# Performance work log

Hardware: AMD Instinct MI355X
Metric: run time of the kernel (lower is better)

The kernel has to match this reference:

```python
import jax, jax.numpy as jnp
import numpy as np

E, B, T = 7, 50, 100               # ensemble (network_size), no_batches=50, time blocks
D, A, L, H, C = 128, 32, 256, 1024, 128  # data, action, latent, hidden, context sizes
H_STEP = 0.1                        # (t1 - t0) / T == dt -> one SDE step per block


def setup_inputs() -> dict:
    key = jax.random.key(0)
    ks = iter(jax.random.split(key, 64))
    def nrm(shape, scale=1.0):
        return jax.random.normal(next(ks), shape, jnp.float32) * scale
    def ens(i, o):
        s = 1.0 / np.sqrt(i)
        return nrm((E, i, o), s), nrm((E, o), s)
    def lin(i, o):
        s = 1.0 / np.sqrt(i)
        return nrm((i, o), s), nrm((o,), s)
    inp = {}
    inp["enc_w1"], inp["enc_b1"] = ens(D, H)
    inp["enc_w2"], inp["enc_b2"] = ens(H, H)
    inp["enc_w3"], inp["enc_b3"] = ens(H, C)
    inp["qz0_w"], inp["qz0_b"] = ens(C, 2 * L)
    inp["act_w"], inp["act_b"] = ens(L + A + D, L)
    inp["proj_w1"], inp["proj_b1"] = ens(L, H)
    inp["proj_w2"], inp["proj_b2"] = ens(H, H)
    inp["proj_w3"], inp["proj_b3"] = ens(H, D)
    inp["f_w1"], inp["f_b1"] = lin(L, H)
    inp["f_w2"], inp["f_b2"] = lin(H, H)
    inp["f_w3"], inp["f_b3"] = lin(H, L)
    inp["h_w1"], inp["h_b1"] = lin(L, H)
    inp["h_w2"], inp["h_b2"] = lin(H, H)
    inp["h_w3"], inp["h_b3"] = lin(H, L)
    # per-latent-dim g nets: Linear(1,H) -> ReLU -> Linear(H,1), stacked over L dims
    inp["g_w1"] = nrm((L, H), 0.2)
    inp["g_b1"] = nrm((L, H), 0.2)
    inp["g_w2"] = nrm((L, H), 0.2 / np.sqrt(H))
    inp["g_b2"] = 0.5 + nrm((L,), 0.01)   # keep diffusion bounded away from 0
    inp["pz0_mean"] = jnp.zeros((E, 1, L), jnp.float32)
    inp["pz0_logstd"] = jnp.zeros((E, 1, L), jnp.float32)
    inp["xs"] = nrm((E, T * B, D))
    inp["actions"] = nrm((E, T * B, A))
    inp["eps_z0"] = nrm((T, E, B, L))      # torch.randn_like noise for z0 reparam
    inp["dw_noise"] = nrm((T, E * B, L))   # Brownian increment noise (unit std)
    return inp


def reference(enc_w1, enc_b1, enc_w2, enc_b2, enc_w3, enc_b3,
              qz0_w, qz0_b, act_w, act_b,
              proj_w1, proj_b1, proj_w2, proj_b2, proj_w3, proj_b3,
              f_w1, f_b1, f_w2, f_b2, f_w3, f_b3,
              h_w1, h_b1, h_w2, h_b2, h_w3, h_b3,
              g_w1, g_b1, g_w2, g_b2,
              pz0_mean, pz0_logstd,
              xs, actions, eps_z0, dw_noise):
    def ens_lin(x, w, b):  # EnsembleFC: bmm + bias
        return jnp.einsum('ebi,eio->ebo', x, w) + b[:, None, :]

    def encoder(x):
        x = jax.nn.relu(ens_lin(x, enc_w1, enc_b1))
        x = jax.nn.relu(ens_lin(x, enc_w2, enc_b2))
        return ens_lin(x, enc_w3, enc_b3)

    def projector(z):
        z = jnp.tanh(ens_lin(z, proj_w1, proj_b1))
        z = jnp.tanh(ens_lin(z, proj_w2, proj_b2))
        return ens_lin(z, proj_w3, proj_b3)

    def mlp(y, w1, b1, w2, b2, w3, b3):  # Linear-ReLU-Linear-Tanh-Linear
        y = jax.nn.relu(y @ w1 + b1)
        y = jnp.tanh(y @ w2 + b2)
        return y @ w3 + b3

    def g_fn(y):  # vectorized per-dim tiny MLPs: y (N, L) -> (N, L)
        hh = jax.nn.relu(y[:, :, None] * g_w1[None] + g_b1[None])  # (N, L, H)
        return jnp.sum(hh * g_w2[None], axis=-1) + g_b2

    xs_t = jnp.moveaxis(xs.reshape(E, T, B, D), 1, 0)        # (T, E, B, D)
    act_t = jnp.moveaxis(actions.reshape(E, T, B, A), 1, 0)  # (T, E, B, A)
    sqrt_h = jnp.sqrt(jnp.float32(H_STEP))

    def step(carry, inps):
        zs_last, i = carry
        x_i, a_i, eps_i, dw_i = inps
        ctx = encoder(x_i)                                  # (E, B, C)
        q = ens_lin(ctx, qz0_w, qz0_b)                      # (E, B, 2L)
        qm, ql = q[..., :L], q[..., L:]
        z0 = qm + jnp.exp(ql) * eps_i
        z_in = jnp.where(i == 0, z0, zs_last)               # first step uses z0
        lad = jnp.concatenate([z_in, a_i, x_i], axis=2)
        z = ens_lin(lad, act_w, act_b).reshape(E * B, L)
        # one SDE step with logqp (f: posterior drift, h: prior drift, g: diffusion)
        fv = mlp(z, f_w1, f_b1, f_w2, f_b2, f_w3, f_b3)
        hv = mlp(z, h_w1, h_b1, h_w2, h_b2, h_w3, h_b3)
        gv = g_fn(z)
        u = (fv - hv) / gv
        lr = 0.5 * jnp.sum(u * u, axis=-1) * H_STEP         # (E*B,) log-ratio increment
        z_new = z + fv * H_STEP + gv * (sqrt_h * dw_i)
        zs_new = z_new.reshape(E, B, L)
        xm = projector(zs_new)                              # (E, B, D)
        # KL(q(z0) || p(z0)) for diagonal Gaussians
        kl = (pz0_logstd - ql) \
             + (jnp.exp(2.0 * ql) + (qm - pz0_mean) ** 2) / (2.0 * jnp.exp(2.0 * pz0_logstd)) \
             - 0.5
        logqp0 = kl.sum(axis=2).mean(axis=1)                # (E,)
        lr_mean = lr.reshape(E, B).mean(axis=1)             # (E,)
        return (zs_new, i + 1), (lr_mean, logqp0, xm)

    init = (jnp.zeros((E, B, L), xs.dtype), jnp.int32(0))
    (_, _), (lrm, lq0, xms) = jax.lax.scan(step, init, (xs_t, act_t, eps_z0, dw_noise))
    logqp_path = lrm.sum(axis=0) + lq0.sum(axis=0)          # (E,)
    predicted_xs = jnp.moveaxis(xms, 0, 1).reshape(E, T * B, D)
    return logqp_path, predicted_xs
```

## Files before the change

kernel.cpp:

```cpp
#include <hip/hip_runtime.h>
#include <hip/hip_bf16.h>
#include <math.h>

#define E_ 7
#define B_ 50
#define T_ 100
#define D_ 128
#define A_ 32
#define L_ 256
#define H_ 1024
#define C_ 128
#define EB_ 350
#define TB_ 5000
#define SQRTH 0.31622776601683794f

typedef __attribute__((ext_vector_type(8))) short s8v;
typedef __attribute__((ext_vector_type(4))) float f32x4;
typedef _Float16 f16x2 __attribute__((ext_vector_type(2)));
typedef __hip_bfloat16 bf16;

#define MFMA __builtin_amdgcn_mfma_f32_16x16x32_bf16

__device__ __forceinline__ int lswz(int row, int ck) {
  return ((ck & ~7) | ((ck ^ row) & 7)) << 3;
}

struct BG {
  const bf16* A[8];
  const bf16* W[8];
  const float* bias[8];
  float* Cf[8];
  bf16* Cb[8];
};

template<int BM, int ACT, int OUT>
__global__ __launch_bounds__(256)
void bgemm(BG g, int M, int K, int lda, int ldw, int ldc) {
  __shared__ short As[BM * 64];
  __shared__ short Ws[128 * 64];
  const short* Ap = (const short*)g.A[blockIdx.z];
  const short* Wp = (const short*)g.W[blockIdx.z];
  const int bm = blockIdx.x * BM, bn = blockIdx.y * 128;
  const int tid = threadIdx.x;
  const int wv = tid >> 6, lane = tid & 63;
  const int wm0 = (wv >> 1) * (BM / 2), wn0 = (wv & 1) * 64;
  const int l15 = lane & 15, l4 = lane >> 4;
  constexpr int FM = BM / 32;
  constexpr int AI = BM / 32;
  f32x4 acc[FM][4] = {};
  for (int k0 = 0; k0 < K; k0 += 64) {
    s8v av[AI], wvv[4];
#pragma unroll
    for (int i = 0; i < AI; ++i) {
      const int c = tid + i * 256, r = c >> 3, ck = c & 7;
      s8v v = {};
      if (bm + r < M) v = *(const s8v*)(Ap + (size_t)(bm + r) * lda + k0 + ck * 8);
      av[i] = v;
    }
#pragma unroll
    for (int i = 0; i < 4; ++i) {
      const int c = tid + i * 256, r = c >> 3, ck = c & 7;
      wvv[i] = *(const s8v*)(Wp + (size_t)(bn + r) * ldw + k0 + ck * 8);
    }
    __syncthreads();
#pragma unroll
    for (int i = 0; i < AI; ++i) {
      const int c = tid + i * 256, r = c >> 3, ck = c & 7;
      *(s8v*)(As + r * 64 + ((ck ^ (r & 7)) << 3)) = av[i];
    }
#pragma unroll
    for (int i = 0; i < 4; ++i) {
      const int c = tid + i * 256, r = c >> 3, ck = c & 7;
      *(s8v*)(Ws + r * 64 + ((ck ^ (r & 7)) << 3)) = wvv[i];
    }
    __syncthreads();
#pragma unroll
    for (int ks = 0; ks < 2; ++ks) {
// ... 68 lines not shown
    ((B4*)d)[i] = o;
  }
}

__global__ __launch_bounds__(256)
void packW(const float* __restrict__ src, bf16* __restrict__ dst, int K, int N) {
  const int idx = blockIdx.x * 256 + threadIdx.x;
  if (idx >= K * N) return;
  const int k = idx / N, n = idx - k * N;
  const size_t fo = ((size_t)(n >> 4) * (K >> 5) + (k >> 5)) * 512 +
                    (((k >> 3) & 3) << 7) + ((n & 15) << 3) + (k & 7);
  dst[fo] = __float2bfloat16(src[idx]);
}

__global__ __launch_bounds__(256)
void packWz(const float* __restrict__ act_w, bf16* __restrict__ hi, bf16* __restrict__ lo) {
  const int idx = blockIdx.x * 256 + threadIdx.x;
  if (idx >= E_ * 65536) return;
  const int e = idx >> 16, rem = idx & 65535, k = rem >> 8, n = rem & 255;
  const float w = act_w[(size_t)e * 416 * 256 + (size_t)k * 256 + n];
  const bf16 h = __float2bfloat16(w);
  const size_t fo = (size_t)e * 65536 + ((size_t)(n >> 4) * 8 + (k >> 5)) * 512 +
                    (((k >> 3) & 3) << 7) + ((n & 15) << 3) + (k & 7);
  hi[fo] = h;
  lo[fo] = __float2bfloat16(w - __bfloat162float(h));
}

__global__ __launch_bounds__(256)
void ax_build(const float* __restrict__ actions, const float* __restrict__ xs,
              bf16* __restrict__ dst) {
  const int idx = blockIdx.x * 256 + threadIdx.x;
  if (idx >= E_ * TB_ * 192) return;
  const int k = idx % 192;
  const int r = (idx / 192) % TB_;
  const int e = idx / (192 * TB_);
  float v = 0.f;
  if (k < 32) v = actions[((size_t)e * TB_ + r) * A_ + k];
  else if (k < 160) v = xs[((size_t)e * TB_ + r) * D_ + (k - 32)];
  dst[idx] = __float2bfloat16(v);
}

__global__ __launch_bounds__(256)
void waxT_build(const float* __restrict__ act_w, bf16* __restrict__ dst) {
  const int idx = blockIdx.x * 256 + threadIdx.x;
  if (idx >= E_ * 256 * 192) return;
  const int k = idx % 192;
  const int n = (idx / 192) % 256;
  const int e = idx / (192 * 256);
  float v = (k < 160) ? act_w[(size_t)e * 416 * 256 + (size_t)(256 + k) * 256 + n] : 0.f;
  dst[idx] = __float2bfloat16(v);
}

__global__ __launch_bounds__(256)
void gpack_build(const float* __restrict__ gw1, const float* __restrict__ gb1,
                 const float* __restrict__ gw2, _Float16* __restrict__ dst) {
  const int idx = blockIdx.x * 256 + threadIdx.x;
  if (idx >= 256 * 3 * 1024) return;
  const int l = idx / 3072, rem = idx - l * 3072, arr = rem >> 10, h = rem & 1023;
  const float* s = arr == 0 ? gw1 : (arr == 1 ? gb1 : gw2);
  dst[idx] = (_Float16)s[(size_t)l * 1024 + h];
}

__global__ __launch_bounds__(256)
void qkl_kernel(const float* __restrict__ ctx, int rows, int row_off, int ctx_estride,
                const float* __restrict__ qw, const float* __restrict__ qb,
                const float* __restrict__ pm, const float* __restrict__ pl,
                const float* __restrict__ eps0, bf16* __restrict__ z0hi,
                bf16* __restrict__ z0lo, float* __restrict__ logqp) {
  __shared__ float cx[16][128];
  __shared__ float red[16];
  const int e = blockIdx.y;
  const int r0 = blockIdx.x * 16;
  const int tid = threadIdx.x;
  {
    const int r = tid >> 4, c = (tid & 15) * 8;
    float4 v0 = make_float4(0.f, 0.f, 0.f, 0.f), v1 = v0;
    if (r0 + r < rows) {
      const float* src = ctx + (size_t)e * ctx_estride + (size_t)(r0 + r) * C_ + c;
      v0 = *(const float4*)src;
      v1 = *(const float4*)(src + 4);
    }
    *(float4*)&cx[r][c] = v0;
    *(float4*)&cx[r][c + 4] = v1;
  }
  if (tid < 16) red[tid] = 0.f;
  __syncthreads();
  const int j = tid;
  const float* w = qw + (size_t)e * C_ * 512;
  float am_[16] = {};
  float al_[16] = {};
  for (int k0 = 0; k0 < C_; k0 += 4) {
    float wm[4], wl[4];
#pragma unroll
    for (int q = 0; q < 4; ++q) {
      wm[q] = w[(size_t)(k0 + q) * 512 + j];
      wl[q] = w[(size_t)(k0 + q) * 512 + 256 + j];
    }
#pragma unroll
    for (int r = 0; r < 16; ++r) {
      const float4 cv = *(const float4*)&cx[r][k0];
      const float cc[4] = {cv.x, cv.y, cv.z, cv.w};
#pragma unroll
      for (int q = 0; q < 4; ++q) {
        am_[r] = fmaf(cc[q], wm[q], am_[r]);
        al_[r] = fmaf(cc[q], wl[q], al_[r]);
      }
    }
  }
  const float qbm = qb[(size_t)e * 512 + j];
  const float qbl = qb[(size_t)e * 512 + 256 + j];
  const float pmv = pm[(size_t)e * L_ + j];
  const float plv = pl[(size_t)e * L_ + j];
  const float inv2e = 0.5f * expf(-2.f * plv);
#pragma unroll
  for (int r = 0; r < 16; ++r) {
    float kl = 0.f;
    if (r0 + r < rows) {
      const float qm_ = am_[r] + qbm;
      const float ql_ = al_[r] + qbl;
      const float dm = qm_ - pmv;
      kl = plv - ql_ + (expf(2.f * ql_) + dm * dm) * inv2e - 0.5f;
      const int gi = row_off + r0 + r;
      if (gi < B_) {
        const size_t zi = ((size_t)e * B_ + gi) * L_ + j;
        const float z0 = qm_ + expf(ql_) * eps0[zi];
        const bf16 h = __float2bfloat16(z0);
        z0hi[zi] = h;
        z0lo[zi] = __float2bfloat16(z0 - __bfloat162float(h));
      }
    }
    for (int off = 32; off; off >>= 1) kl += __shfl_xor(kl, off, 64);
    if ((tid & 63) == 0) atomicAdd(&red[r], kl);
  }
  __syncthreads();
  if (tid < 16 && r0 + tid < rows) atomicAdd(&logqp[e], red[tid] * (1.0f / B_));
}

__global__ __launch_bounds__(256, 2)
void k1_act(const bf16* __restrict__ zhi, const bf16* __restrict__ zlo,
            const bf16* __restrict__ wzh, const bf16* __restrict__ wzl,
            const float* __restrict__ axw, float* __restrict__ zP,
            bf16* __restrict__ zPb, int t) {
  __shared__ short Ah[16 * 256];
  __shared__ short Al[16 * 256];
  const int e = blockIdx.z, rb = blockIdx.x, nb = blockIdx.y * 128;
  const int r0 = rb * 13;
  const int nrows = (50 - r0 < 13) ? (50 - r0) : 13;
  const int tid = threadIdx.x, lane = tid & 63, wv = tid >> 6;
  const int l15 = lane & 15, l4 = lane >> 4;
  const short* zh = (const short*)zhi + (size_t)(e * 50 + r0) * 256;
  const short* zl = (const short*)zlo + (size_t)(e * 50 + r0) * 256;
#pragma unroll
  for (int i = 0; i < 2; ++i) {
    const int lin = tid + i * 256, row = lin >> 5, ck = lin & 31;
    s8v vh = {}, vl = {};
    if (row < nrows) {
      vh = *(const s8v*)(zh + row * 256 + ck * 8);
      vl = *(const s8v*)(zl + row * 256 + ck * 8);
    }
    *(s8v*)(Ah + row * 256 + lswz(row, ck)) = vh;
    *(s8v*)(Al + row * 256 + lswz(row, ck)) = vl;
  }
  __syncthreads();
  const short* Bh = (const short*)wzh + (size_t)e * 65536;
  const short* Bl = (const short*)wzl + (size_t)e * 65536;
  f32x4 acc[2] = {};
#pragma unroll
  for (int kt = 0; kt < 8; ++kt) {
    const int ck = kt * 4 + l4;
    const s8v ah = *(const s8v*)(Ah + l15 * 256 + lswz(l15, ck));
    const s8v al = *(const s8v*)(Al + l15 * 256 + lswz(l15, ck));
#pragma unroll
    for (int nt = 0; nt < 2; ++nt) {
      const int ng = nb + wv * 32 + nt * 16;
      const size_t bo = ((size_t)(ng >> 4) * 8 + kt) * 512 + lane * 8;
      const s8v bh = *(const s8v*)(Bh + bo);
      const s8v bl = *(const s8v*)(Bl + bo);
      acc[nt] = MFMA(ah, bh, acc[nt], 0, 0, 0);
      acc[nt] = MFMA(al, bh, acc[nt], 0, 0, 0);
      acc[nt] = MFMA(ah, bl, acc[nt], 0, 0, 0);
    }
  }
#pragma unroll
  for (int nt = 0; nt < 2; ++nt) {
    const int col = nb + wv * 32 + nt * 16 + l15;
#pragma unroll
    for (int j = 0; j < 4; ++j) {
      const int row = l4 * 4 + j;
      if (row < nrows) {
        const int gr = e * 50 + r0 + row;
        const float v = acc[nt][j] + axw[((size_t)e * TB_ + t * 50 + r0 + row) * 256 + col];
        zP[(size_t)gr * 256 + col] = v;
        zPb[(size_t)gr * 256 + col] = __float2bfloat16(v);
      }
    }
  }
}

__global__ __launch_bounds__(256, 2)
void k2_l1(const bf16* __restrict__ zPb, const bf16* __restrict__ w1f,
           const float* __restrict__ fb1, const float* __restrict__ hb1,
           bf16* __restrict__ fh1) {
  __shared__ short As[16 * 256];
  const int rb = blockIdx.x, nb = blockIdx.y * 128;
  const int r0 = rb * 16;
  const int tid = threadIdx.x, lane = tid & 63, wv = tid >> 6;
  const int l15 = lane & 15, l4 = lane >> 4;
#pragma unroll
  for (int i = 0; i < 2; ++i) {
    const int lin = tid + i * 256, row = lin >> 5, ck = lin & 31;
    s8v v = {};
    if (r0 + row < EB_)
      v = *(const s8v*)((const short*)zPb + (size_t)(r0 + row) * 256 + ck * 8);
    *(s8v*)(As + row * 256 + lswz(row, ck)) = v;
  }
  __syncthreads();
  f32x4 acc[2] = {};
#pragma unroll
  for (int kt = 0; kt < 8; ++kt) {
    const int ck = kt * 4 + l4;
    const s8v a = *(const s8v*)(As + l15 * 256 + lswz(l15, ck));
#pragma unroll
    for (int nt = 0; nt < 2; ++nt) {
      const int ng = nb + wv * 32 + nt * 16;
      const s8v b = *(const s8v*)((const short*)w1f + ((size_t)(ng >> 4) * 8 + kt) * 512 + lane * 8);
      acc[nt] = MFMA(a, b, acc[nt], 0, 0, 0);
    }
  }
#pragma unroll
  for (int nt = 0; nt < 2; ++nt) {
    const int col = nb + wv * 32 + nt * 16 + l15;
    const float bv = (col < 1024) ? fb1[col] : hb1[col - 1024];
#pragma unroll
    for (int j = 0; j < 4; ++j) {
      const int row = r0 + l4 * 4 + j;
      if (row < EB_)
        fh1[(size_t)row * 2048 + col] = __float2bfloat16(fmaxf(acc[nt][j] + bv, 0.f));
    }
  }
}

__global__ __launch_bounds__(256, 2)
void k3_l2(const bf16* __restrict__ fh1, const bf16* __restrict__ w2f,
           const float* __restrict__ fb2, const float* __restrict__ hb2,
           bf16* __restrict__ fh2) {
  __shared__ short As[16 * 1024];
  const int rb = blockIdx.x, nbl = blockIdx.y;
  const int nb = nbl * 128, r0 = rb * 16;
  const int half = (nbl >= 8) ? 1024 : 0;
  const int tid = threadIdx.x, lane = tid & 63, wv = tid >> 6;
  const int l15 = lane & 15, l4 = lane >> 4;
#pragma unroll
  for (int i = 0; i < 8; ++i) {
    const int lin = tid + i * 256, row = lin >> 7, ck = lin & 127;
    s8v v = {};
    if (r0 + row < EB_)
      v = *(const s8v*)((const short*)fh1 + (size_t)(r0 + row) * 2048 + half + ck * 8);
    *(s8v*)(As + row * 1024 + lswz(row, ck)) = v;
  }
  __syncthreads();
  f32x4 acc[2] = {};
#pragma unroll 4
  for (int kt = 0; kt < 32; ++kt) {
    const int ck = kt * 4 + l4;
    const s8v a = *(const s8v*)(As + l15 * 1024 + lswz(l15, ck));
#pragma unroll
    for (int nt = 0; nt < 2; ++nt) {
      const int ng = nb + wv * 32 + nt * 16;
      const s8v b = *(const s8v*)((const short*)w2f + ((size_t)(ng >> 4) * 32 + kt) * 512 + lane * 8);
      acc[nt] = MFMA(a, b, acc[nt], 0, 0, 0);
    }
  }
#pragma unroll
  for (int nt = 0; nt < 2; ++nt) {
    const int col = nb + wv * 32 + nt * 16 + l15;
    const float bv = half ? hb2[col - 1024] : fb2[col];
#pragma unroll
    for (int j = 0; j < 4; ++j) {
      const int row = r0 + l4 * 4 + j;
      if (row < EB_)
        fh2[(size_t)row * 2048 + col] = __float2bfloat16(tanhf(acc[nt][j] + bv));
    }
  }
}

__global__ __launch_bounds__(256, 1)
void k4_fin(const bf16* __restrict__ fh2, const bf16* __restrict__ w3f,
            const float* __restrict__ fb3, const float* __restrict__ hb3,
            const _Float16* __restrict__ gpk, const float* __restrict__ gb2,
            const float* __restrict__ zP, const float* __restrict__ dw,
            bf16* __restrict__ zhi, bf16* __restrict__ zlo,
            bf16* __restrict__ zs_bf, float* __restrict__ logqp, int t) {
  __shared__ short As[16 * 1024];
  __shared__ float ztile[16][64];
  __shared__ float gvt[16][64];
  __shared__ float ebuck[8];
  const int rb = blockIdx.x, cb = blockIdx.y;
  const int r0 = rb * 16, c0 = cb * 64;
  const int tid = threadIdx.x, lane = tid & 63, wv = tid >> 6;
  const int l15 = lane & 15, l4 = lane >> 4;
  if (tid < 8) ebuck[tid] = 0.f;
#pragma unroll
  for (int i = 0; i < 4; ++i) {
    const int lin = tid + i * 256, row = lin >> 6, col = lin & 63;
    ztile[row][col] = (r0 + row < EB_) ? zP[(size_t)(r0 + row) * 256 + c0 + col] : 1.0f;
  }
  f32x4 accF = {}, accH = {};
#pragma unroll
  for (int fb = 0; fb < 2; ++fb) {
    __syncthreads();
#pragma unroll
    for (int i = 0; i < 8; ++i) {
      const int lin = tid + i * 256, row = lin >> 7, ck = lin & 127;
      s8v v = {};
      if (r0 + row < EB_)
        v = *(const s8v*)((const short*)fh2 + (size_t)(r0 + row) * 2048 + fb * 1024 + ck * 8);
      *(s8v*)(As + row * 1024 + lswz(row, ck)) = v;
    }
    __syncthreads();
    const int ng = fb * 256 + c0 + wv * 16;
    f32x4 acc = {};
#pragma unroll 4
    for (int kt = 0; kt < 32; ++kt) {
      const int ck = kt * 4 + l4;
      const s8v a = *(const s8v*)(As + l15 * 1024 + lswz(l15, ck));
      const s8v b = *(const s8v*)((const short*)w3f + ((size_t)(ng >> 4) * 32 + kt) * 512 + lane * 8);
      acc = MFMA(a, b, acc, 0, 0, 0);
    }
    if (fb) accH = acc; else accF = acc;
  }
  __syncthreads();
  {
    const int lloc = tid >> 2, hq = tid & 3;
    const _Float16* gl = gpk + (size_t)(c0 + lloc) * 3072 + hq * 256;
    f16x2 z2[16];
#pragma unroll
    for (int r = 0; r < 16; ++r) {
      const _Float16 zh_ = (_Float16)ztile[r][lloc];
      z2[r] = f16x2{zh_, zh_};
    }
    float ga[16] = {};
    for (int hp = 0; hp < 128; ++hp) {
      const f16x2 w1v = *(const f16x2*)(gl + 2 * hp);
      const f16x2 b1v = *(const f16x2*)(gl + 1024 + 2 * hp);
      const f16x2 w2v = *(const f16x2*)(gl + 2048 + 2 * hp);
#pragma unroll
      for (int r = 0; r < 16; ++r) {
        f16x2 tt = z2[r] * w1v + b1v;
#if __has_builtin(__builtin_elementwise_max)
        const f16x2 zz = {};
        tt = __builtin_elementwise_max(tt, zz);
#else
        tt[0] = tt[0] > (_Float16)0 ? tt[0] : (_Float16)0;
        tt[1] = tt[1] > (_Float16)0 ? tt[1] : (_Float16)0;
#endif
#if __has_builtin(__builtin_amdgcn_fdot2)
        ga[r] = __builtin_amdgcn_fdot2(tt, w2v, ga[r], false);
#else
        ga[r] += (float)tt[0] * (float)w2v[0] + (float)tt[1] * (float)w2v[1];
#endif
      }
    }
#pragma unroll
    for (int r = 0; r < 16; ++r) {
      float v = ga[r];
      v += __shfl_xor(v, 1, 64);
      v += __shfl_xor(v, 2, 64);
      if (hq == 0) gvt[r][lloc] = v + gb2[c0 + lloc];
    }
  }
  __syncthreads();
  const int col_loc = wv * 16 + l15, col = c0 + col_loc;
  const float fb3v = fb3[col], hb3v = hb3[col];
#pragma unroll
  for (int j = 0; j < 4; ++j) {
    const int rl = l4 * 4 + j, row = r0 + rl;
    if (row < EB_) {
      const float fv = accF[j] + fb3v;
      const float hv = accH[j] + hb3v;
      const float gv = gvt[rl][col_loc];
      const float u = (fv - hv) / gv;
      atomicAdd(&ebuck[row / 50], 0.001f * u * u);
      const float znew = ztile[rl][col_loc] + 0.1f * fv +
                         gv * (SQRTH * dw[(size_t)t * (EB_ * 256) + (size_t)row * 256 + col]);
      const bf16 h = __float2bfloat16(znew);
      const size_t zi = (size_t)row * 256 + col;
      zhi[zi] = h;
      zlo[zi] = __float2bfloat16(znew - __bfloat162float(h));
      const int e = row / 50, b = row - e * 50;
      zs_bf[((size_t)e * TB_ + t * 50 + b) * 256 + col] = h;
    }
  }
  __syncthreads();
  if (tid < 7) {
    const float v = ebuck[tid];
    if (v != 0.f) atomicAdd(&logqp[tid], v);
  }
}

__global__ void init_kernel(float* logqp) {
  if (threadIdx.x < E_) logqp[threadIdx.x] = 0.f;
}

extern "C" void kernel_launch(void* const* d_in, const int* in_sizes, int n_in,
                              void* d_out, int out_size, void* d_ws, size_t ws_size,
                              hipStream_t stream) {
  (void)in_sizes; (void)n_in; (void)out_size;
  const float* enc_w1 = (const float*)d_in[0];
  const float* enc_b1 = (const float*)d_in[1];
  const float* enc_w2 = (const float*)d_in[2];
  const float* enc_b2 = (const float*)d_in[3];
  const float* enc_w3 = (const float*)d_in[4];
  const float* enc_b3 = (const float*)d_in[5];
  const float* qz0_w  = (const float*)d_in[6];
  const float* qz0_b  = (const float*)d_in[7];
  const float* act_w  = (const float*)d_in[8];
  const float* act_b  = (const float*)d_in[9];
  const float* proj_w1 = (const float*)d_in[10];
  const float* proj_b1 = (const float*)d_in[11];
  const float* proj_w2 = (const float*)d_in[12];
  const float* proj_b2 = (const float*)d_in[13];
  const float* proj_w3 = (const float*)d_in[14];
  const float* proj_b3 = (const float*)d_in[15];
  const float* f_w1 = (const float*)d_in[16];
  const float* f_b1 = (const float*)d_in[17];
  const float* f_w2 = (const float*)d_in[18];
  const float* f_b2 = (const float*)d_in[19];
  const float* f_w3 = (const float*)d_in[20];
  const float* f_b3 = (const float*)d_in[21];
  const float* h_w1 = (const float*)d_in[22];
  const float* h_b1 = (const float*)d_in[23];
  const float* h_w2 = (const float*)d_in[24];
  const float* h_b2 = (const float*)d_in[25];
  const float* h_w3 = (const float*)d_in[26];
  const float* h_b3 = (const float*)d_in[27];
  const float* g_w1 = (const float*)d_in[28];
  const float* g_b1 = (const float*)d_in[29];
  const float* g_w2 = (const float*)d_in[30];
  const float* g_b2 = (const float*)d_in[31];
  const float* pz0_mean   = (const float*)d_in[32];
  const float* pz0_logstd = (const float*)d_in[33];
  const float* xs      = (const float*)d_in[34];
  const float* actions = (const float*)d_in[35];
  const float* eps_z0  = (const float*)d_in[36];
  const float* dw      = (const float*)d_in[37];

  float* out = (float*)d_out;
  float* logqp = out;
  float* pred = out + E_;

  char* base = (char*)d_ws;
  size_t off = 0;
  auto alloc = [&](size_t bytes) {
    void* p = base + off;
    off = (off + bytes + 255) & ~(size_t)255;
    return p;
  };
  bf16* zhi    = (bf16*)alloc((size_t)EB_ * 256 * 2);
  bf16* zlo    = (bf16*)alloc((size_t)EB_ * 256 * 2);
  float* zP    = (float*)alloc((size_t)EB_ * 256 * 4);
  bf16* zPb    = (bf16*)alloc((size_t)EB_ * 256 * 2);
  bf16* fh1    = (bf16*)alloc((size_t)EB_ * 2048 * 2);
  bf16* fh2    = (bf16*)alloc((size_t)EB_ * 2048 * 2);
  bf16* zs_bf  = (bf16*)alloc((size_t)E_ * T_ * B_ * 256 * 2);
  float* axw   = (float*)alloc((size_t)E_ * TB_ * 256 * 4);
  bf16* ax_bf  = (bf16*)alloc((size_t)E_ * TB_ * 192 * 2);
  bf16* waxT   = (bf16*)alloc((size_t)E_ * 256 * 192 * 2);
  bf16* wzh    = (bf16*)alloc((size_t)E_ * 65536 * 2);
  bf16* wzl    = (bf16*)alloc((size_t)E_ * 65536 * 2);
  bf16* w1f    = (bf16*)alloc((size_t)2048 * 256 * 2);
  bf16* w2f    = (bf16*)alloc((size_t)2048 * 1024 * 2);
  bf16* w3f    = (bf16*)alloc((size_t)512 * 1024 * 2);
  _Float16* gpk = (_Float16*)alloc((size_t)256 * 3 * 1024 * 2);
  bf16* xs_bf  = (bf16*)alloc((size_t)E_ * TB_ * D_ * 2);
  bf16* ew1T = (bf16*)alloc((size_t)E_ * D_ * H_ * 2);
  bf16* ew2T = (bf16*)alloc((size_t)E_ * H_ * H_ * 2);
  bf16* ew3T = (bf16*)alloc((size_t)E_ * H_ * C_ * 2);
  bf16* pw1T = (bf16*)alloc((size_t)E_ * L_ * H_ * 2);
  bf16* pw2T = (bf16*)alloc((size_t)E_ * H_ * H_ * 2);
  bf16* pw3T = (bf16*)alloc((size_t)E_ * H_ * D_ * 2);
  const size_t per_row = (size_t)E_ * (H_ * 2 * 2 + C_ * 4);
  size_t remain = (ws_size > off + 4096) ? (ws_size - off - 4096) : 0;
  int CH = (int)(remain / per_row);
  if (CH > 2500) CH = 2500;
  if (CH < 64) CH = 64;
  bf16* bufA = (bf16*)alloc((size_t)E_ * CH * H_ * 2);
  bf16* bufB = (bf16*)alloc((size_t)E_ * CH * H_ * 2);
  float* bufC = (float*)alloc((size_t)E_ * CH * C_ * 4);

  init_kernel<<<dim3(1), dim3(64), 0, stream>>>(logqp);

  const dim3 cb256(256);
  cvt_kernel<<<dim3((E_ * TB_ * D_ / 4 + 255) / 256), cb256, 0, stream>>>(xs, xs_bf, E_ * TB_ * D_ / 4);
  cvtT_kernel<<<dim3(H_ / 32, D_ / 32, E_), cb256, 0, stream>>>(enc_w1, ew1T, D_, H_, (long)D_ * H_, (long)D_ * H_);
  cvtT_kernel<<<dim3(H_ / 32, H_ / 32, E_), cb256, 0, stream>>>(enc_w2, ew2T, H_, H_, (long)H_ * H_, (long)H_ * H_);
  cvtT_kernel<<<dim3(C_ / 32, H_ / 32, E_), cb256, 0, stream>>>(enc_w3, ew3T, H_, C_, (long)H_ * C_, (long)H_ * C_);
  cvtT_kernel<<<dim3(H_ / 32, L_ / 32, E_), cb256, 0, stream>>>(proj_w1, pw1T, L_, H_, (long)L_ * H_, (long)L_ * H_);
  cvtT_kernel<<<dim3(H_ / 32, H_ / 32, E_), cb256, 0, stream>>>(proj_w2, pw2T, H_, H_, (long)H_ * H_, (long)H_ * H_);
  cvtT_kernel<<<dim3(D_ / 32, H_ / 32, E_), cb256, 0, stream>>>(proj_w3, pw3T, H_, D_, (long)H_ * D_, (long)H_ * D_);
  ax_build<<<dim3((E_ * TB_ * 192 + 255) / 256), cb256, 0, stream>>>(actions, xs, ax_bf);
  waxT_build<<<dim3((E_ * 256 * 192 + 255) / 256), cb256, 0, stream>>>(act_w, waxT);
  packWz<<<dim3((E_ * 65536 + 255) / 256), cb256, 0, stream>>>(act_w, wzh, wzl);
  packW<<<dim3((256 * 1024 + 255) / 256), cb256, 0, stream>>>(f_w1, w1f, 256, 1024);
  packW<<<dim3((256 * 1024 + 255) / 256), cb256, 0, stream>>>(h_w1, w1f + (size_t)1024 * 256, 256, 1024);
  packW<<<dim3((1024 * 1024 + 255) / 256), cb256, 0, stream>>>(f_w2, w2f, 1024, 1024);
  packW<<<dim3((1024 * 1024 + 255) / 256), cb256, 0, stream>>>(h_w2, w2f + (size_t)1024 * 1024, 1024, 1024);
  packW<<<dim3((1024 * 256 + 255) / 256), cb256, 0, stream>>>(f_w3, w3f, 1024, 256);
  packW<<<dim3((1024 * 256 + 255) / 256), cb256, 0, stream>>>(h_w3, w3f + (size_t)256 * 1024, 1024, 256);
  gpack_build<<<dim3((256 * 3 * 1024 + 255) / 256), cb256, 0, stream>>>(g_w1, g_b1, g_w2, gpk);

  BG g;
  for (int e = 0; e < E_; ++e) {
    g.A[e] = ax_bf + (size_t)e * TB_ * 192;
    g.W[e] = waxT + (size_t)e * 256 * 192;
    g.bias[e] = act_b + (size_t)e * 256;
    g.Cf[e] = axw + (size_t)e * TB_ * 256;
  }
  bgemm<128, 0, 0><<<dim3((TB_ + 127) / 128, 2, E_), 256, 0, stream>>>(g, TB_, 192, 192, 192, 256);

  for (int c = 0; c < TB_; c += CH) {
    const int rows = (TB_ - c < CH) ? (TB_ - c) : CH;
    const int mt = (rows + 127) / 128;
    for (int e = 0; e < E_; ++e) {
      g.A[e] = xs_bf + ((size_t)e * TB_ + c) * D_;
      g.W[e] = ew1T + (size_t)e * D_ * H_;
      g.bias[e] = enc_b1 + (size_t)e * H_;
      g.Cb[e] = bufA + (size_t)e * CH * H_;
    }
    bgemm<128, 1, 1><<<dim3(mt, H_ / 128, E_), 256, 0, stream>>>(g, rows, D_, D_, D_, H_);
    for (int e = 0; e < E_; ++e) {
      g.A[e] = bufA + (size_t)e * CH * H_;
      g.W[e] = ew2T + (size_t)e * H_ * H_;
      g.bias[e] = enc_b2 + (size_t)e * H_;
      g.Cb[e] = bufB + (size_t)e * CH * H_;
    }
    bgemm<128, 1, 1><<<dim3(mt, H_ / 128, E_), 256, 0, stream>>>(g, rows, H_, H_, H_, H_);
    for (int e = 0; e < E_; ++e) {
      g.A[e] = bufB + (size_t)e * CH * H_;
      g.W[e] = ew3T + (size_t)e * H_ * C_;
      g.bias[e] = enc_b3 + (size_t)e * C_;
      g.Cf[e] = bufC + (size_t)e * CH * C_;
    }
    bgemm<128, 0, 0><<<dim3(mt, C_ / 128, E_), 256, 0, stream>>>(g, rows, H_, H_, H_, C_);
    qkl_kernel<<<dim3((rows + 15) / 16, E_), 256, 0, stream>>>(
        bufC, rows, c, CH * C_, qz0_w, qz0_b, pz0_mean, pz0_logstd, eps_z0,
        zhi, zlo, logqp);
  }

  for (int t = 0; t < T_; ++t) {
    k1_act<<<dim3(4, 2, E_), 256, 0, stream>>>(zhi, zlo, wzh, wzl, axw, zP, zPb, t);
    k2_l1<<<dim3(22, 16), 256, 0, stream>>>(zPb, w1f, f_b1, h_b1, fh1);
    k3_l2<<<dim3(22, 16), 256, 0, stream>>>(fh1, w2f, f_b2, h_b2, fh2);
    k4_fin<<<dim3(22, 4), 256, 0, stream>>>(fh2, w3f, f_b3, h_b3, gpk, g_b2,
                                            zP, dw, zhi, zlo, zs_bf, logqp, t);
  }

  for (int c = 0; c < TB_; c += CH) {
    const int rows = (TB_ - c < CH) ? (TB_ - c) : CH;
    const int mt = (rows + 127) / 128;
    for (int e = 0; e < E_; ++e) {
      g.A[e] = zs_bf + ((size_t)e * T_ * B_ + c) * L_;
      g.W[e] = pw1T + (size_t)e * L_ * H_;
      g.bias[e] = proj_b1 + (size_t)e * H_;
      g.Cb[e] = bufA + (size_t)e * CH * H_;
    }
    bgemm<128, 2, 1><<<dim3(mt, H_ / 128, E_), 256, 0, stream>>>(g, rows, L_, L_, L_, H_);
    for (int e = 0; e < E_; ++e) {
      g.A[e] = bufA + (size_t)e * CH * H_;
      g.W[e] = pw2T + (size_t)e * H_ * H_;
      g.bias[e] = proj_b2 + (size_t)e * H_;
      g.Cb[e] = bufB + (size_t)e * CH * H_;
    }
    bgemm<128, 2, 1><<<dim3(mt, H_ / 128, E_), 256, 0, stream>>>(g, rows, H_, H_, H_, H_);
    for (int e = 0; e < E_; ++e) {
      g.A[e] = bufB + (size_t)e * CH * H_;
      g.W[e] = pw3T + (size_t)e * H_ * D_;
      g.bias[e] = proj_b3 + (size_t)e * D_;
      g.Cf[e] = pred + ((size_t)e * TB_ + c) * D_;
    }
    bgemm<128, 0, 0><<<dim3(mt, D_ / 128, E_), 256, 0, stream>>>(g, rows, H_, H_, H_, D_);
  }
}
```

Baseline: 10.30 ms.

## Fuse SDE time loop into single persistent kernel with warp-specialized g-net

The 400 per-step launches (act, layer1, layer2, final) are replaced by one persistent kernel of 28 workgroups, one per ensemble member and batch quarter, which keeps the latent state in LDS across all 100 steps. Eight waves run the f and h MLPs on MFMA while the other eight compute the per-dimension g-net in fp16 concurrently. The g weights are repacked for coalesced access, and the z state is held in fp32 in LDS instead of being written back to global as hi/lo bf16 each step. This removes launch overhead and global round-trips, at the cost of using only 28 CUs and each workgroup re-streaming the full f/h weights from cache every step.

```diff
diff --git a/kernel.cpp b/kernel.cpp
--- a/kernel.cpp
+++ b/kernel.cpp
@@ -22,7 +22,28 @@
 #define MFMA __builtin_amdgcn_mfma_f32_16x16x32_bf16
 
 __device__ __forceinline__ int lswz(int row, int ck) {
-  return ((ck & ~7) | ((ck ^ row) & 7)) << 3;
+  return (((ck & ~7) | ((ck ^ row) & 7)) << 3);
+}
+__device__ __forceinline__ int swzE(int r, int col) {
+  const int ck = col >> 3;
+  return (((ck & ~7) | ((ck ^ r) & 7)) << 3) + (col & 7);
+}
+__device__ __forceinline__ f16x2 relu2(f16x2 t) {
+#if __has_builtin(__builtin_elementwise_max)
+  const f16x2 zz = {};
+  return __builtin_elementwise_max(t, zz);
+#else
+  t[0] = t[0] > (_Float16)0 ? t[0] : (_Float16)0;
+  t[1] = t[1] > (_Float16)0 ? t[1] : (_Float16)0;
+  return t;
+#endif
+}
+__device__ __forceinline__ float fdot2a(f16x2 a, f16x2 b, float c) {
+#if __has_builtin(__builtin_amdgcn_fdot2)
+  return __builtin_amdgcn_fdot2(a, b, c, false);
+#else
+  return c + (float)a[0] * (float)b[0] + (float)a[1] * (float)b[1];
+#endif
 }
 
 struct BG {
@@ -197,21 +218,24 @@
 }
 
 __global__ __launch_bounds__(256)
-void gpack_build(const float* __restrict__ gw1, const float* __restrict__ gb1,
-                 const float* __restrict__ gw2, _Float16* __restrict__ dst) {
+void gpack2(const float* __restrict__ gw1, const float* __restrict__ gb1,
+            const float* __restrict__ gw2, _Float16* __restrict__ dst) {
   const int idx = blockIdx.x * 256 + threadIdx.x;
-  if (idx >= 256 * 3 * 1024) return;
-  const int l = idx / 3072, rem = idx - l * 3072, arr = rem >> 10, h = rem & 1023;
+  if (idx >= 3 * 512 * 256 * 2) return;
+  const int i = idx & 1;
+  const int l = (idx >> 1) & 255;
+  const int hpg = (idx >> 9) & 511;
+  const int arr = idx >> 18;
   const float* s = arr == 0 ? gw1 : (arr == 1 ? gb1 : gw2);
-  dst[idx] = (_Float16)s[(size_t)l * 1024 + h];
+  dst[idx] = (_Float16)s[(size_t)l * 1024 + hpg * 2 + i];
 }
 
 __global__ __launch_bounds__(256)
 void qkl_kernel(const float* __restrict__ ctx, int rows, int row_off, int ctx_estride,
                 const float* __restrict__ qw, const float* __restrict__ qb,
                 const float* __restrict__ pm, const float* __restrict__ pl,
-                const float* __restrict__ eps0, bf16* __restrict__ z0hi,
-                bf16* __restrict__ z0lo, float* __restrict__ logqp) {
+                const float* __restrict__ eps0, float* __restrict__ z0f,
+                float* __restrict__ logqp) {
   __shared__ float cx[16][128];
   __shared__ float red[16];
   const int e = blockIdx.y;
@@ -268,10 +292,7 @@
       const int gi = row_off + r0 + r;
       if (gi < B_) {
         const size_t zi = ((size_t)e * B_ + gi) * L_ + j;
-        const float z0 = qm_ + expf(ql_) * eps0[zi];
-        const bf16 h = __float2bfloat16(z0);
-        z0hi[zi] = h;
-        z0lo[zi] = __float2bfloat16(z0 - __bfloat162float(h));
+        z0f[zi] = qm_ + expf(ql_) * eps0[zi];
       }
     }
     for (int off = 32; off; off >>= 1) kl += __shfl_xor(kl, off, 64);
@@ -281,265 +302,258 @@
   if (tid < 16 && r0 + tid < rows) atomicAdd(&logqp[e], red[tid] * (1.0f / B_));
 }
 
-__global__ __launch_bounds__(256, 2)
-void k1_act(const bf16* __restrict__ zhi, const bf16* __restrict__ zlo,
-            const bf16* __restrict__ wzh, const bf16* __restrict__ wzl,
-            const float* __restrict__ axw, float* __restrict__ zP,
-            bf16* __restrict__ zPb, int t) {
-  __shared__ short Ah[16 * 256];
-  __shared__ short Al[16 * 256];
-  const int e = blockIdx.z, rb = blockIdx.x, nb = blockIdx.y * 128;
-  const int r0 = rb * 13;
-  const int nrows = (50 - r0 < 13) ? (50 - r0) : 13;
-  const int tid = threadIdx.x, lane = tid & 63, wv = tid >> 6;
+struct SC {
+  const bf16 *wzh, *wzl, *w1f, *w2f, *w3f;
+  const _Float16* gpk;
+  const float *fb1, *hb1, *fb2, *hb2, *fb3, *hb3, *gb2;
+  const float *axw, *dw, *z0f;
+  bf16* zs_bf;
+  float* logqp;
+};
+
+template<int KT, int NT>
+__device__ __forceinline__ void mm(const short* As_, int astride, const short* Bf,
+                                   int ngBase, int lane, f32x4* acc) {
   const int l15 = lane & 15, l4 = lane >> 4;
-  const short* zh = (const short*)zhi + (size_t)(e * 50 + r0) * 256;
-  const short* zl = (const short*)zlo + (size_t)(e * 50 + r0) * 256;
-#pragma unroll
-  for (int i = 0; i < 2; ++i) {
-    const int lin = tid + i * 256, row = lin >> 5, ck = lin & 31;
-    s8v vh = {}, vl = {};
-    if (row < nrows) {
-      vh = *(const s8v*)(zh + row * 256 + ck * 8);
-      vl = *(const s8v*)(zl + row * 256 + ck * 8);
-    }
-    *(s8v*)(Ah + row * 256 + lswz(row, ck)) = vh;
-    *(s8v*)(Al + row * 256 + lswz(row, ck)) = vl;
+#pragma unroll 4
+  for (int kt = 0; kt < KT; ++kt) {
+    const s8v av = *(const s8v*)(As_ + l15 * astride + lswz(l15, kt * 4 + l4));
+#pragma unroll
+    for (int nt = 0; nt < NT; ++nt) {
+      const s8v bv = *(const s8v*)(Bf + ((size_t)((ngBase + nt) * KT + kt)) * 512 + lane * 8);
+      acc[nt] = MFMA(av, bv, acc[nt], 0, 0, 0);
+    }
+  }
+}
+
+__global__ __launch_bounds__(1024, 4) void scan28(SC a) {
+  __shared__ float zst[16 * 256];
+  __shared__ float zP[16 * 256];
+  __shared__ float fvb[16 * 256];
+  __shared__ float gvt[16 * 256];
+  __shared__ short zPb[16 * 256];
+  __shared__ short zh_[16 * 256];
+  __shared__ short zl_[16 * 256];
+  __shared__ short S[16 * 1024];
+  __shared__ short S2[16 * 1024];
+  const int wg = blockIdx.x;
+  const int e = wg >> 2, q = wg & 3;
+  const int nr = (q < 2) ? 13 : 12;
+  const int b0 = (q < 2) ? q * 13 : 26 + (q - 2) * 12;
+  const int tid = threadIdx.x;
+  const int wave = tid >> 6, lane = tid & 63, l15 = lane & 15, l4 = lane >> 4;
+  const int mw = wave & 7;
+  const bool isM = wave < 8;
+  const int gt = (wave - 8) * 64 + lane;
+  const int gl = gt >> 1, ghh = gt & 1;
+
+  for (int i = tid; i < 4096; i += 1024) {
+    const int r = i >> 8, c = i & 255;
+    zst[i] = (r < nr) ? a.z0f[(size_t)((e * 50 + b0 + r) * 256 + c)] : 0.f;
+  }
+  float lrA = 0.f;
+  const short* wzhE = (const short*)a.wzh + (size_t)e * 65536;
+  const short* wzlE = (const short*)a.wzl + (size_t)e * 65536;
+  const short* w1p = (const short*)a.w1f;
+  const short* w2p = (const short*)a.w2f;
+  const short* w3p = (const short*)a.w3f;
+
+  for (int t = 0; t < T_; ++t) {
+    __syncthreads();
+    for (int i = tid; i < 4096; i += 1024) {
+      const int r = i >> 8, c = i & 255;
+      const float f = zst[i];
+      const bf16 h = __float2bfloat16(f);
+      const bf16 lo = __float2bfloat16(f - __bfloat162float(h));
+      const int eo = r * 256 + swzE(r, c);
+      *(bf16*)&zh_[eo] = h;
+      *(bf16*)&zl_[eo] = lo;
+    }
+    __syncthreads();
+    {
+      f32x4 acc = {};
+#pragma unroll
+      for (int kt = 0; kt < 8; ++kt) {
+        const s8v ah = *(const s8v*)(zh_ + l15 * 256 + lswz(l15, kt * 4 + l4));
+        const s8v al = *(const s8v*)(zl_ + l15 * 256 + lswz(l15, kt * 4 + l4));
+        const size_t bo = ((size_t)(wave * 8 + kt)) * 512 + lane * 8;
+        const s8v bh = *(const s8v*)(wzhE + bo);
+        const s8v bl = *(const s8v*)(wzlE + bo);
+        acc = MFMA(ah, bh, acc, 0, 0, 0);
+        acc = MFMA(al, bh, acc, 0, 0, 0);
+        acc = MFMA(ah, bl, acc, 0, 0, 0);
+      }
+      const int col = wave * 16 + l15;
+#pragma unroll
+      for (int j = 0; j < 4; ++j) {
+        const int r = l4 * 4 + j;
+        float v = 0.f;
+        if (r < nr)
+          v = acc[j] + a.axw[((size_t)(e * TB_) + t * 50 + b0 + r) * 256 + col];
+        zP[r * 256 + col] = v;
+        *(bf16*)&zPb[r * 256 + swzE(r, col)] = __float2bfloat16(v);
+      }
+    }
+    __syncthreads();
+
+    f16x2 z2g[13];
+    float ga[13];
+    if (!isM) {
+#pragma unroll
+      for (int r = 0; r < 13; ++r) {
+        const _Float16 zh2 = (_Float16)zP[r * 256 + gl];
+        z2g[r] = f16x2{zh2, zh2};
+        ga[r] = 0.f;
+      }
+    }
+    auto gchunk = [&](int h0, int h1) {
+      for (int hp = h0; hp < h1; ++hp) {
+        const size_t o = ((size_t)(ghh * 256 + hp)) * 512 + gl * 2;
+        const f16x2 w1 = *(const f16x2*)(a.gpk + o);
+        const f16x2 b1 = *(const f16x2*)(a.gpk + 262144 + o);
+        const f16x2 w2 = *(const f16x2*)(a.gpk + 524288 + o);
+#pragma unroll
+        for (int r = 0; r < 13; ++r)
+          ga[r] = fdot2a(relu2(z2g[r] * w1 + b1), w2, ga[r]);
+      }
+    };
+
+    if (isM) {
+#pragma unroll
+      for (int ph = 0; ph < 2; ++ph) {
+        f32x4 acc[4] = {};
+        mm<8, 4>(zPb, 256, w1p, mw * 8 + ph * 4, lane, acc);
+#pragma unroll
+        for (int nt = 0; nt < 4; ++nt) {
+          const int col = (mw * 8 + ph * 4 + nt) * 16 + l15;
+          const float bv = a.fb1[col];
+#pragma unroll
+          for (int j = 0; j < 4; ++j) {
+            const int r = l4 * 4 + j;
+            *(bf16*)&S[r * 1024 + swzE(r, col)] =
+                __float2bfloat16(fmaxf(acc[nt][j] + bv, 0.f));
+          }
+        }
+      }
+    } else gchunk(0, 24);
+    __syncthreads();
+    if (isM) {
+#pragma unroll
+      for (int ph = 0; ph < 2; ++ph) {
+        f32x4 acc[4] = {};
+        mm<32, 4>(S, 1024, w2p, mw * 8 + ph * 4, lane, acc);
+#pragma unroll
+        for (int nt = 0; nt < 4; ++nt) {
+          const int col = (mw * 8 + ph * 4 + nt) * 16 + l15;
+          const float bv = a.fb2[col];
+#pragma unroll
+          for (int j = 0; j < 4; ++j) {
+            const int r = l4 * 4 + j;
+            *(bf16*)&S2[r * 1024 + swzE(r, col)] =
+                __float2bfloat16(tanhf(acc[nt][j] + bv));
+          }
+        }
+      }
+    } else gchunk(24, 104);
+    __syncthreads();
+    if (isM) {
+      f32x4 acc[2] = {};
+      mm<32, 2>(S2, 1024, w3p, mw * 2, lane, acc);
+#pragma unroll
+      for (int nt = 0; nt < 2; ++nt) {
+        const int col = (mw * 2 + nt) * 16 + l15;
+        const float bv = a.fb3[col];
+#pragma unroll
+        for (int j = 0; j < 4; ++j)
+          fvb[(l4 * 4 + j) * 256 + col] = acc[nt][j] + bv;
+      }
+    } else gchunk(104, 128);
+    __syncthreads();
+    if (isM) {
+#pragma unroll
+      for (int ph = 0; ph < 2; ++ph) {
+        f32x4 acc[4] = {};
+        mm<8, 4>(zPb, 256, w1p, 64 + mw * 8 + ph * 4, lane, acc);
+#pragma unroll
+        for (int nt = 0; nt < 4; ++nt) {
+          const int col = (mw * 8 + ph * 4 + nt) * 16 + l15;
+          const float bv = a.hb1[col];
+#pragma unroll
+          for (int j = 0; j < 4; ++j) {
+            const int r = l4 * 4 + j;
+            *(bf16*)&S[r * 1024 + swzE(r, col)] =
+                __float2bfloat16(fmaxf(acc[nt][j] + bv, 0.f));
+          }
+        }
+      }
+    } else gchunk(128, 152);
+    __syncthreads();
+    if (isM) {
+#pragma unroll
+      for (int ph = 0; ph < 2; ++ph) {
+        f32x4 acc[4] = {};
+        mm<32, 4>(S, 1024, w2p, 64 + mw * 8 + ph * 4, lane, acc);
+#pragma unroll
+        for (int nt = 0; nt < 4; ++nt) {
+          const int col = (mw * 8 + ph * 4 + nt) * 16 + l15;
+          const float bv = a.hb2[col];
+#pragma unroll
+          for (int j = 0; j < 4; ++j) {
+            const int r = l4 * 4 + j;
+            *(bf16*)&S2[r * 1024 + swzE(r, col)] =
+                __float2bfloat16(tanhf(acc[nt][j] + bv));
+          }
+        }
+      }
+    } else gchunk(152, 232);
+    __syncthreads();
+    f32x4 acc3[2] = {};
+    if (isM) {
+      mm<32, 2>(S2, 1024, w3p, 16 + mw * 2, lane, acc3);
+    } else {
+      gchunk(232, 256);
+#pragma unroll
+      for (int r = 0; r < 13; ++r) {
+        const float v = ga[r] + __shfl_xor(ga[r], 1, 64);
+        if (ghh == 0) gvt[r * 256 + gl] = v + a.gb2[gl];
+      }
+    }
+    __syncthreads();
+    if (isM) {
+#pragma unroll
+      for (int nt = 0; nt < 2; ++nt) {
+        const int col = (mw * 2 + nt) * 16 + l15;
+        const float hb = a.hb3[col];
+#pragma unroll
+        for (int j = 0; j < 4; ++j) {
+          const int r = l4 * 4 + j;
+          if (r < nr) {
+            const float fv = fvb[r * 256 + col];
+            const float hv = acc3[nt][j] + hb;
+            const float gv = gvt[r * 256 + col];
+            const float u = (fv - hv) / gv;
+            lrA += u * u;
+            const float zn = zP[r * 256 + col] + 0.1f * fv +
+                gv * (SQRTH * a.dw[(size_t)t * (EB_ * 256) +
+                                   (size_t)((e * 50 + b0 + r) * 256 + col)]);
+            zst[r * 256 + col] = zn;
+            a.zs_bf[((size_t)(e * TB_) + t * 50 + b0 + r) * 256 + col] =
+                __float2bfloat16(zn);
+          }
+        }
+      }
+    }
   }
   __syncthreads();
-  const short* Bh = (const short*)wzh + (size_t)e * 65536;
-  const short* Bl = (const short*)wzl + (size_t)e * 65536;
-  f32x4 acc[2] = {};
-#pragma unroll
-  for (int kt = 0; kt < 8; ++kt) {
-    const int ck = kt * 4 + l4;
-    const s8v ah = *(const s8v*)(Ah + l15 * 256 + lswz(l15, ck));
-    const s8v al = *(const s8v*)(Al + l15 * 256 + lswz(l15, ck));
-#pragma unroll
-    for (int nt = 0; nt < 2; ++nt) {
-      const int ng = nb + wv * 32 + nt * 16;
-      const size_t bo = ((size_t)(ng >> 4) * 8 + kt) * 512 + lane * 8;
-      const s8v bh = *(const s8v*)(Bh + bo);
-      const s8v bl = *(const s8v*)(Bl + bo);
-      acc[nt] = MFMA(ah, bh, acc[nt], 0, 0, 0);
-      acc[nt] = MFMA(al, bh, acc[nt], 0, 0, 0);
-      acc[nt] = MFMA(ah, bl, acc[nt], 0, 0, 0);
-    }
-  }
-#pragma unroll
-  for (int nt = 0; nt < 2; ++nt) {
-    const int col = nb + wv * 32 + nt * 16 + l15;
-#pragma unroll
-    for (int j = 0; j < 4; ++j) {
-      const int row = l4 * 4 + j;
-      if (row < nrows) {
-        const int gr = e * 50 + r0 + row;
-        const float v = acc[nt][j] + axw[((size_t)e * TB_ + t * 50 + r0 + row) * 256 + col];
-        zP[(size_t)gr * 256 + col] = v;
-        zPb[(size_t)gr * 256 + col] = __float2bfloat16(v);
-      }
-    }
-  }
-}
-
-__global__ __launch_bounds__(256, 2)
-void k2_l1(const bf16* __restrict__ zPb, const bf16* __restrict__ w1f,
-           const float* __restrict__ fb1, const float* __restrict__ hb1,
-           bf16* __restrict__ fh1) {
-  __shared__ short As[16 * 256];
-  const int rb = blockIdx.x, nb = blockIdx.y * 128;
-  const int r0 = rb * 16;
-  const int tid = threadIdx.x, lane = tid & 63, wv = tid >> 6;
-  const int l15 = lane & 15, l4 = lane >> 4;
-#pragma unroll
-  for (int i = 0; i < 2; ++i) {
-    const int lin = tid + i * 256, row = lin >> 5, ck = lin & 31;
-    s8v v = {};
-    if (r0 + row < EB_)
-      v = *(const s8v*)((const short*)zPb + (size_t)(r0 + row) * 256 + ck * 8);
-    *(s8v*)(As + row * 256 + lswz(row, ck)) = v;
-  }
+  float v = lrA;
+#pragma unroll
+  for (int o = 32; o; o >>= 1) v += __shfl_xor(v, o, 64);
+  if (lane == 0) gvt[wave] = v;
   __syncthreads();
-  f32x4 acc[2] = {};
-#pragma unroll
-  for (int kt = 0; kt < 8; ++kt) {
-    const int ck = kt * 4 + l4;
-    const s8v a = *(const s8v*)(As + l15 * 256 + lswz(l15, ck));
-#pragma unroll
-    for (int nt = 0; nt < 2; ++nt) {
-      const int ng = nb + wv * 32 + nt * 16;
-      const s8v b = *(const s8v*)((const short*)w1f + ((size_t)(ng >> 4) * 8 + kt) * 512 + lane * 8);
-      acc[nt] = MFMA(a, b, acc[nt], 0, 0, 0);
-    }
-  }
-#pragma unroll
-  for (int nt = 0; nt < 2; ++nt) {
-    const int col = nb + wv * 32 + nt * 16 + l15;
-    const float bv = (col < 1024) ? fb1[col] : hb1[col - 1024];
-#pragma unroll
-    for (int j = 0; j < 4; ++j) {
-      const int row = r0 + l4 * 4 + j;
-      if (row < EB_)
-        fh1[(size_t)row * 2048 + col] = __float2bfloat16(fmaxf(acc[nt][j] + bv, 0.f));
-    }
-  }
-}
-
-__global__ __launch_bounds__(256, 2)
-void k3_l2(const bf16* __restrict__ fh1, const bf16* __restrict__ w2f,
-           const float* __restrict__ fb2, const float* __restrict__ hb2,
-           bf16* __restrict__ fh2) {
-  __shared__ short As[16 * 1024];
-  const int rb = blockIdx.x, nbl = blockIdx.y;
-  const int nb = nbl * 128, r0 = rb * 16;
-  const int half = (nbl >= 8) ? 1024 : 0;
-  const int tid = threadIdx.x, lane = tid & 63, wv = tid >> 6;
-  const int l15 = lane & 15, l4 = lane >> 4;
-#pragma unroll
-  for (int i = 0; i < 8; ++i) {
-    const int lin = tid + i * 256, row = lin >> 7, ck = lin & 127;
-    s8v v = {};
-    if (r0 + row < EB_)
-      v = *(const s8v*)((const short*)fh1 + (size_t)(r0 + row) * 2048 + half + ck * 8);
-    *(s8v*)(As + row * 1024 + lswz(row, ck)) = v;
-  }
-  __syncthreads();
-  f32x4 acc[2] = {};
-#pragma unroll 4
-  for (int kt = 0; kt < 32; ++kt) {
-    const int ck = kt * 4 + l4;
-    const s8v a = *(const s8v*)(As + l15 * 1024 + lswz(l15, ck));
-#pragma unroll
-    for (int nt = 0; nt < 2; ++nt) {
-      const int ng = nb + wv * 32 + nt * 16;
-      const s8v b = *(const s8v*)((const short*)w2f + ((size_t)(ng >> 4) * 32 + kt) * 512 + lane * 8);
-      acc[nt] = MFMA(a, b, acc[nt], 0, 0, 0);
-    }
-  }
-#pragma unroll
-  for (int nt = 0; nt < 2; ++nt) {
-    const int col = nb + wv * 32 + nt * 16 + l15;
-    const float bv = half ? hb2[col - 1024] : fb2[col];
-#pragma unroll
-    for (int j = 0; j < 4; ++j) {
-      const int row = r0 + l4 * 4 + j;
-      if (row < EB_)
-        fh2[(size_t)row * 2048 + col] = __float2bfloat16(tanhf(acc[nt][j] + bv));
-    }
-  }
-}
-
-__global__ __launch_bounds__(256, 1)
-void k4_fin(const bf16* __restrict__ fh2, const bf16* __restrict__ w3f,
-            const float* __restrict__ fb3, const float* __restrict__ hb3,
-            const _Float16* __restrict__ gpk, const float* __restrict__ gb2,
-            const float* __restrict__ zP, const float* __restrict__ dw,
-            bf16* __restrict__ zhi, bf16* __restrict__ zlo,
-            bf16* __restrict__ zs_bf, float* __restrict__ logqp, int t) {
-  __shared__ short As[16 * 1024];
-  __shared__ float ztile[16][64];
-  __shared__ float gvt[16][64];
-  __shared__ float ebuck[8];
-  const int rb = blockIdx.x, cb = blockIdx.y;
-  const int r0 = rb * 16, c0 = cb * 64;
-  const int tid = threadIdx.x, lane = tid & 63, wv = tid >> 6;
-  const int l15 = lane & 15, l4 = lane >> 4;
-  if (tid < 8) ebuck[tid] = 0.f;
-#pragma unroll
-  for (int i = 0; i < 4; ++i) {
-    const int lin = tid + i * 256, row = lin >> 6, col = lin & 63;
-    ztile[row][col] = (r0 + row < EB_) ? zP[(size_t)(r0 + row) * 256 + c0 + col] : 1.0f;
-  }
-  f32x4 accF = {}, accH = {};
-#pragma unroll
-  for (int fb = 0; fb < 2; ++fb) {
-    __syncthreads();
-#pragma unroll
-    for (int i = 0; i < 8; ++i) {
-      const int lin = tid + i * 256, row = lin >> 7, ck = lin & 127;
-      s8v v = {};
-      if (r0 + row < EB_)
-        v = *(const s8v*)((const short*)fh2 + (size_t)(r0 + row) * 2048 + fb * 1024 + ck * 8);
-      *(s8v*)(As + row * 1024 + lswz(row, ck)) = v;
-    }
-    __syncthreads();
-    const int ng = fb * 256 + c0 + wv * 16;
-    f32x4 acc = {};
-#pragma unroll 4
-    for (int kt = 0; kt < 32; ++kt) {
-      const int ck = kt * 4 + l4;
-      const s8v a = *(const s8v*)(As + l15 * 1024 + lswz(l15, ck));
-      const s8v b = *(const s8v*)((const short*)w3f + ((size_t)(ng >> 4) * 32 + kt) * 512 + lane * 8);
-      acc = MFMA(a, b, acc, 0, 0, 0);
-    }
-    if (fb) accH = acc; else accF = acc;
-  }
-  __syncthreads();
-  {
-    const int lloc = tid >> 2, hq = tid & 3;
-    const _Float16* gl = gpk + (size_t)(c0 + lloc) * 3072 + hq * 256;
-    f16x2 z2[16];
-#pragma unroll
-    for (int r = 0; r < 16; ++r) {
-      const _Float16 zh_ = (_Float16)ztile[r][lloc];
-      z2[r] = f16x2{zh_, zh_};
-    }
-    float ga[16] = {};
-    for (int hp = 0; hp < 128; ++hp) {
-      const f16x2 w1v = *(const f16x2*)(gl + 2 * hp);
-      const f16x2 b1v = *(const f16x2*)(gl + 1024 + 2 * hp);
-      const f16x2 w2v = *(const f16x2*)(gl + 2048 + 2 * hp);
-#pragma unroll
-      for (int r = 0; r < 16; ++r) {
-        f16x2 tt = z2[r] * w1v + b1v;
-#if __has_builtin(__builtin_elementwise_max)
-        const f16x2 zz = {};
-        tt = __builtin_elementwise_max(tt, zz);
-#else
-        tt[0] = tt[0] > (_Float16)0 ? tt[0] : (_Float16)0;
-        tt[1] = tt[1] > (_Float16)0 ? tt[1] : (_Float16)0;
-#endif
-#if __has_builtin(__builtin_amdgcn_fdot2)
-        ga[r] = __builtin_amdgcn_fdot2(tt, w2v, ga[r], false);
-#else
-        ga[r] += (float)tt[0] * (float)w2v[0] + (float)tt[1] * (float)w2v[1];
-#endif
-      }
-    }
-#pragma unroll
-    for (int r = 0; r < 16; ++r) {
-      float v = ga[r];
-      v += __shfl_xor(v, 1, 64);
-      v += __shfl_xor(v, 2, 64);
-      if (hq == 0) gvt[r][lloc] = v + gb2[c0 + lloc];
-    }
-  }
-  __syncthreads();
-  const int col_loc = wv * 16 + l15, col = c0 + col_loc;
-  const float fb3v = fb3[col], hb3v = hb3[col];
-#pragma unroll
-  for (int j = 0; j < 4; ++j) {
-    const int rl = l4 * 4 + j, row = r0 + rl;
-    if (row < EB_) {
-      const float fv = accF[j] + fb3v;
-      const float hv = accH[j] + hb3v;
-      const float gv = gvt[rl][col_loc];
-      const float u = (fv - hv) / gv;
-      atomicAdd(&ebuck[row / 50], 0.001f * u * u);
-      const float znew = ztile[rl][col_loc] + 0.1f * fv +
-                         gv * (SQRTH * dw[(size_t)t * (EB_ * 256) + (size_t)row * 256 + col]);
-      const bf16 h = __float2bfloat16(znew);
-      const size_t zi = (size_t)row * 256 + col;
-      zhi[zi] = h;
-      zlo[zi] = __float2bfloat16(znew - __bfloat162float(h));
-      const int e = row / 50, b = row - e * 50;
-      zs_bf[((size_t)e * TB_ + t * 50 + b) * 256 + col] = h;
-    }
-  }
-  __syncthreads();
-  if (tid < 7) {
-    const float v = ebuck[tid];
-    if (v != 0.f) atomicAdd(&logqp[tid], v);
+  if (tid == 0) {
+    float s = 0.f;
+    for (int w = 0; w < 16; ++w) s += gvt[w];
+    atomicAdd(&a.logqp[e], 0.001f * s);
   }
 }
 
@@ -601,12 +615,7 @@
     off = (off + bytes + 255) & ~(size_t)255;
     return p;
   };
-  bf16* zhi    = (bf16*)alloc((size_t)EB_ * 256 * 2);
-  bf16* zlo    = (bf16*)alloc((size_t)EB_ * 256 * 2);
-  float* zP    = (float*)alloc((size_t)EB_ * 256 * 4);
-  bf16* zPb    = (bf16*)alloc((size_t)EB_ * 256 * 2);
-  bf16* fh1    = (bf16*)alloc((size_t)EB_ * 2048 * 2);
-  bf16* fh2    = (bf16*)alloc((size_t)EB_ * 2048 * 2);
+  float* z0f   = (float*)alloc((size_t)EB_ * 256 * 4);
   bf16* zs_bf  = (bf16*)alloc((size_t)E_ * T_ * B_ * 256 * 2);
   float* axw   = (float*)alloc((size_t)E_ * TB_ * 256 * 4);
   bf16* ax_bf  = (bf16*)alloc((size_t)E_ * TB_ * 192 * 2);
@@ -616,7 +625,7 @@
   bf16* w1f    = (bf16*)alloc((size_t)2048 * 256 * 2);
   bf16* w2f    = (bf16*)alloc((size_t)2048 * 1024 * 2);
   bf16* w3f    = (bf16*)alloc((size_t)512 * 1024 * 2);
-  _Float16* gpk = (_Float16*)alloc((size_t)256 * 3 * 1024 * 2);
+  _Float16* gpk = (_Float16*)alloc((size_t)3 * 512 * 256 * 2 * 2);
   bf16* xs_bf  = (bf16*)alloc((size_t)E_ * TB_ * D_ * 2);
   bf16* ew1T = (bf16*)alloc((size_t)E_ * D_ * H_ * 2);
   bf16* ew2T = (bf16*)alloc((size_t)E_ * H_ * H_ * 2);
@@ -652,7 +661,7 @@
   packW<<<dim3((1024 * 1024 + 255) / 256), cb256, 0, stream>>>(h_w2, w2f + (size_t)1024 * 1024, 1024, 1024);
   packW<<<dim3((1024 * 256 + 255) / 256), cb256, 0, stream>>>(f_w3, w3f, 1024, 256);
   packW<<<dim3((1024 * 256 + 255) / 256), cb256, 0, stream>>>(h_w3, w3f + (size_t)256 * 1024, 1024, 256);
-  gpack_build<<<dim3((256 * 3 * 1024 + 255) / 256), cb256, 0, stream>>>(g_w1, g_b1, g_w2, gpk);
+  gpack2<<<dim3((3 * 512 * 256 * 2 + 255) / 256), cb256, 0, stream>>>(g_w1, g_b1, g_w2, gpk);
 
   BG g;
   for (int e = 0; e < E_; ++e) {
@@ -689,16 +698,17 @@
     bgemm<128, 0, 0><<<dim3(mt, C_ / 128, E_), 256, 0, stream>>>(g, rows, H_, H_, H_, C_);
     qkl_kernel<<<dim3((rows + 15) / 16, E_), 256, 0, stream>>>(
         bufC, rows, c, CH * C_, qz0_w, qz0_b, pz0_mean, pz0_logstd, eps_z0,
-        zhi, zlo, logqp);
-  }
-
-  for (int t = 0; t < T_; ++t) {
-    k1_act<<<dim3(4, 2, E_), 256, 0, stream>>>(zhi, zlo, wzh, wzl, axw, zP, zPb, t);
-    k2_l1<<<dim3(22, 16), 256, 0, stream>>>(zPb, w1f, f_b1, h_b1, fh1);
-    k3_l2<<<dim3(22, 16), 256, 0, stream>>>(fh1, w2f, f_b2, h_b2, fh2);
-    k4_fin<<<dim3(22, 4), 256, 0, stream>>>(fh2, w3f, f_b3, h_b3, gpk, g_b2,
-                                            zP, dw, zhi, zlo, zs_bf, logqp, t);
-  }
+        z0f, logqp);
+  }
+
+  SC sc;
+  sc.wzh = wzh; sc.wzl = wzl; sc.w1f = w1f; sc.w2f = w2f; sc.w3f = w3f;
+  sc.gpk = gpk;
+  sc.fb1 = f_b1; sc.hb1 = h_b1; sc.fb2 = f_b2; sc.hb2 = h_b2;
+  sc.fb3 = f_b3; sc.hb3 = h_b3; sc.gb2 = g_b2;
+  sc.axw = axw; sc.dw = dw; sc.z0f = z0f;
+  sc.zs_bf = zs_bf; sc.logqp = logqp;
+  scan28<<<dim3(28), dim3(1024), 0, stream>>>(sc);
 
   for (int c = 0; c < TB_; c += CH) {
     const int rows = (TB_ - c < CH) ? (TB_ - c) : CH;
```

Measured after the change: 29.09 ms. +182.6%, slower.
